# Kernel tuning notes

Hardware: AMD Instinct MI355X
Metric: run time of the kernel (lower is better)

## Reference

```python
import jax, jax.numpy as jnp
import numpy as np

N_USER = 100000
N_ITEM = 50000
N_EDGE = 400000
D_IN = 128
N_HEADS = 4
D_HEAD = 32


def setup_inputs() -> dict:
    key = jax.random.key(0)
    ks = jax.random.split(key, 10)
    s = 1.0 / np.sqrt(D_IN)
    return {
        "h_user": jax.random.normal(ks[0], (N_USER, D_IN), jnp.float32),
        "h_item": jax.random.normal(ks[1], (N_ITEM, D_IN), jnp.float32),
        "edge_user": jax.random.randint(ks[2], (N_EDGE,), 0, N_USER),
        "edge_item": jax.random.randint(ks[3], (N_EDGE,), 0, N_ITEM),
        "user_w_qs": jax.random.normal(ks[4], (N_HEADS, D_IN, D_HEAD), jnp.float32) * s,
        "user_w_ks": jax.random.normal(ks[5], (N_HEADS, D_IN, D_HEAD), jnp.float32) * s,
        "user_w_vs": jax.random.normal(ks[6], (N_HEADS, D_IN, D_HEAD), jnp.float32) * s,
        "item_w_qs": jax.random.normal(ks[7], (N_HEADS, D_IN, D_HEAD), jnp.float32) * s,
        "item_w_ks": jax.random.normal(ks[8], (N_HEADS, D_IN, D_HEAD), jnp.float32) * s,
        "item_w_vs": jax.random.normal(ks[9], (N_HEADS, D_IN, D_HEAD), jnp.float32) * s,
    }


def _segment_softmax(logit, seg, num_segments):
    m = jax.ops.segment_max(logit, seg, num_segments=num_segments)
    e = jnp.exp(logit - m[seg])
    s = jax.ops.segment_sum(e, seg, num_segments=num_segments)
    return e / s[seg]


def _attend(src_idx, dst_idx, h_src, h_dst, w_qs, w_ks, w_vs, n_dst):
    # per-head projections: [H, n, d_head]
    q = jnp.einsum("nd,hde->hne", h_dst, w_qs)
    k = jnp.einsum("nd,hde->hne", h_src, w_ks)
    v = jnp.einsum("nd,hde->hne", h_src, w_vs)
    # per-edge logits: [H, E]
    logit = jnp.sum(q[:, dst_idx] * k[:, src_idx], axis=-1)
    att = jax.vmap(lambda l: _segment_softmax(l, dst_idx, n_dst))(logit)
    # sparse adj @ v == segment-sum of attention-weighted source values
    msg = att[..., None] * v[:, src_idx]  # [H, E, d_head]
    z = jax.vmap(lambda m: jax.ops.segment_sum(m, dst_idx, num_segments=n_dst))(msg)
    z = jax.nn.relu(z)  # nonlinear per head, then merge (concat)
    return jnp.transpose(z, (1, 0, 2)).reshape(n_dst, -1)


def reference(h_user, h_item, edge_user, edge_item,
              user_w_qs, user_w_ks, user_w_vs,
              item_w_qs, item_w_ks, item_w_vs):
    # i2u: items -> users (dst = users)
    z_user = _attend(edge_item, edge_user, h_item, h_user,
                     user_w_qs, item_w_ks, item_w_vs, N_USER)
    # u2i: users -> items (dst = items)
    z_item = _attend(edge_user, edge_item, h_user, h_item,
                     item_w_qs, user_w_ks, user_w_vs, N_ITEM)
    return (z_user, z_item)
```

## Files before the change

kernel.cpp:

```cpp
#include <hip/hip_runtime.h>
#include <hip/hip_fp16.h>


typedef unsigned short u16;
typedef float f32x4 __attribute__((ext_vector_type(4)));
typedef short bf16x8 __attribute__((ext_vector_type(8)));

#define NU_C    100000
#define NI_C    50000
#define E_C     400000
#define D_IN    128
#define D_HEAD  32
#define N_HEADS 4

#define RBU 3125
#define RBI 1563
#define WU  (3 * RBU)
#define WI  (3 * RBI)
#define WT_BLKS 384

#define SCAN_T  256
#define SCAN_E  1024

__device__ __forceinline__ float bf2f(u16 b) {
    return __uint_as_float(((unsigned)b) << 16);
}

__device__ __forceinline__ u16 f2bf_rn(float x) {
    unsigned u = __float_as_uint(x);
    u += 0x7FFFu + ((u >> 16) & 1u);
    return (u16)(u >> 16);
}

__device__ __forceinline__ u16 f2h(float x) {
    return __half_as_ushort(__float2half(x));
}
__device__ __forceinline__ float h2f(u16 b) {
    return __half2float(__ushort_as_half(b));
}

__global__ void detect_dtypes(const void* __restrict__ h,
                              const void* __restrict__ eu,
                              int* __restrict__ flags) {
    int t = threadIdx.x;
    const u16* hw = (const u16*)h;
    int cnt = 0;
#pragma unroll
    for (int r = 0; r < 2; ++r) {
        int i = t + r * 64;
        unsigned ex = (hw[2 * i] >> 7) & 0xFFu;
        if (ex >= 118u && ex <= 137u) cnt++;
    }
    const int* ew = (const int*)eu;
    int nz = 0;
#pragma unroll
    for (int r = 0; r < 4; ++r) {
        int i = t + r * 64;
        if (ew[2 * i + 1] != 0) nz++;
    }
#pragma unroll
    for (int m = 1; m < 64; m <<= 1) {
        cnt += __shfl_xor(cnt, m);
        nz  += __shfl_xor(nz, m);
    }
    if (t == 0) {
        flags[0] = (cnt >= 64) ? 1 : 0;
        flags[1] = (nz == 0) ? 1 : 0;
        flags[2] = 0;
        flags[3] = 0;
    }
}

__global__ __launch_bounds__(256)
void prep(const void* __restrict__ w0, const void* __restrict__ w1,
          const void* __restrict__ w2, const void* __restrict__ w3,
          const void* __restrict__ w4, const void* __restrict__ w5,
          u16* __restrict__ wthi, u16* __restrict__ wtlo,
          const int* __restrict__ e_user, const int* __restrict__ e_item,
          int* __restrict__ du, int* __restrict__ di,
          int* __restrict__ degU, int* __restrict__ degI,
          int* __restrict__ flags) {
    int b = blockIdx.x;
    if (b < WT_BLKS) {
        int m = b >> 6;
        int f = (b & 63) * 256 + threadIdx.x;
        const void* ws[6] = { w0, w1, w2, w3, w4, w5 };
        const void* wp = ws[m];
        int head = f >> 12, e = f & 31;
        float x;
        if (flags[0]) x = bf2f(((const u16*)wp)[f]);
        else          x = ((const float*)wp)[f];
        u16 h = f2bf_rn(x);
        u16 l = f2bf_rn(x - bf2f(h));
        int o = m * 16384 + (head * 32 + e) * 128 + ((f >> 5) & 127);
        wthi[o] = h;
        wtlo[o] = l;
    } else {
        int g = (b - WT_BLKS) * 256 + threadIdx.x;
        if (g >= E_C) return;
        int is64 = flags[1];
        int u = is64 ? e_user[2 * g] : e_user[g];
        int i = is64 ? e_item[2 * g] : e_item[g];
        if ((unsigned)u >= (unsigned)NU_C) { atomicOr(&flags[3], 1); u = 0; }
        if ((unsigned)i >= (unsigned)NI_C) { atomicOr(&flags[3], 1); i = 0; }
        du[g] = u;
        di[g] = i;
        atomicAdd(&degU[u], 1);
        atomicAdd(&degI[i], 1);
    }
}

__global__ __launch_bounds__(SCAN_T)
void scan_pass1(const int* __restrict__ degU, int* __restrict__ offsU,
                int* __restrict__ partU, int nU, int sbU,
                const int* __restrict__ degI, int* __restrict__ offsI,
                int* __restrict__ partI, int nI) {
    __shared__ int tsum[SCAN_T];
    int t = threadIdx.x, b = blockIdx.x;
    const int* deg; int* offs; int* partials; int n; int lb;
    if (b < sbU) { deg = degU; offs = offsU; partials = partU; n = nU; lb = b; }
    else         { deg = degI; offs = offsI; partials = partI; n = nI; lb = b - sbU; }
    int idx = lb * SCAN_E + t * 4;
    int v0 = 0, v1 = 0, v2 = 0, v3 = 0;
    if (idx + 3 < n) {
        v0 = deg[idx]; v1 = deg[idx + 1]; v2 = deg[idx + 2]; v3 = deg[idx + 3];
    } else {
        if (idx     < n) v0 = deg[idx];
        if (idx + 1 < n) v1 = deg[idx + 1];
        if (idx + 2 < n) v2 = deg[idx + 2];
        if (idx + 3 < n) v3 = deg[idx + 3];
    }
    int s = v0 + v1 + v2 + v3;
    tsum[t] = s;
    __syncthreads();
#pragma unroll
    for (int o = 1; o < SCAN_T; o <<= 1) {
        int x = (t >= o) ? tsum[t - o] : 0;
        __syncthreads();
        tsum[t] += x;
        __syncthreads();
    }
    int run = tsum[t] - s;
    if (idx     < n) offs[idx]     = run;             run += v0;
    if (idx + 1 < n) offs[idx + 1] = run;             run += v1;
    if (idx + 2 < n) offs[idx + 2] = run;             run += v2;
    if (idx + 3 < n) offs[idx + 3] = run;
    if (t == SCAN_T - 1) partials[lb] = tsum[t];
}

__global__ __launch_bounds__(SCAN_T)
void scan_pass2(int* __restrict__ partU, int sbU,
                int* __restrict__ partI, int sbI) {
    __shared__ int tsum[SCAN_T];
    int t = threadIdx.x;
    int* partials; int nb;
    if (blockIdx.x == 0) { partials = partU; nb = sbU; }
    else                 { partials = partI; nb = sbI; }
    int v = (t < nb) ? partials[t] : 0;
    tsum[t] = v;
    __syncthreads();
#pragma unroll
    for (int o = 1; o < SCAN_T; o <<= 1) {
        int x = (t >= o) ? tsum[t - o] : 0;
        __syncthreads();
        tsum[t] += x;
        __syncthreads();
    }
    if (t < nb) partials[t] = tsum[t] - v;
}

__global__ void scatter2(const int* __restrict__ du, const int* __restrict__ di,
                         const int* __restrict__ offsU, const int* __restrict__ partU,
                         int* __restrict__ cntU, int* __restrict__ csrU,
                         const int* __restrict__ offsI, const int* __restrict__ partI,
                         int* __restrict__ cntI, int* __restrict__ csrI, int egrid) {
    int b = blockIdx.x;
    int g = (b >= egrid ? b - egrid : b) * 256 + threadIdx.x;
    if (g >= E_C) return;
    if (b < egrid) {
        int d = du[g];
        int pos = offsU[d] + partU[d >> 10] + atomicAdd(&cntU[d], 1);
        csrU[pos] = di[g];
    } else {
        int d = di[g];
        int pos = offsI[d] + partI[d >> 10] + atomicAdd(&cntI[d], 1);
        csrI[pos] = du[g];
    }
}

__global__ __launch_bounds__(256)
void projw(const void* __restrict__ hu, const void* __restrict__ hi_,
           const u16* __restrict__ wthi_, const u16* __restrict__ wtlo_,
           u16* __restrict__ QU, u16* __restrict__ KU, u16* __restrict__ VU,
           u16* __restrict__ QI, u16* __restrict__ KI, u16* __restrict__ VI,
           const int* __restrict__ flags) {
    int wid = blockIdx.x * 4 + (threadIdx.x >> 6);
    int l = threadIdx.x & 63;
    const int lr = l & 15, lk = l >> 4;

    const void* hraw; const u16* wth; const u16* wtl; u16* out; int N; int rb;
    if (wid < WU) {
        int m = wid / RBU; rb = wid - m * RBU;
        hraw = hu; N = NU_C;
        wth = wthi_ + m * 16384; wtl = wtlo_ + m * 16384;
        out = (m == 0) ? QU : ((m == 1) ? KU : VU);
    } else {
        int w2 = wid - WU;
        int m = w2 / RBI; rb = w2 - m * RBI;
        hraw = hi_; N = NI_C;
        wth = wthi_ + (3 + m) * 16384; wtl = wtlo_ + (3 + m) * 16384;
        out = (m == 0) ? QI : ((m == 1) ? KI : VI);
    }

    const int n0 = rb * 32;
    const int row0 = min(n0 + lr, N - 1);
    const int row1 = min(n0 + 16 + lr, N - 1);
    const int isbf = flags[0];

    f32x4 acc[2][8];
#pragma unroll
    for (int rt = 0; rt < 2; ++rt)
#pragma unroll
        for (int ct = 0; ct < 8; ++ct) {
            acc[rt][ct].x = 0.f; acc[rt][ct].y = 0.f;
            acc[rt][ct].z = 0.f; acc[rt][ct].w = 0.f;
        }

#pragma unroll
    for (int kc = 0; kc < 4; ++kc) {
        const int kof = kc * 32 + lk * 8;
        bf16x8 fAh[2], fAl[2];
        if (!isbf) {
            const float* hp = (const float*)hraw;
#pragma unroll
            for (int rt = 0; rt < 2; ++rt) {
                const float* a = hp + (size_t)(rt ? row1 : row0) * D_IN + kof;
                f32x4 a0 = *(const f32x4*)a;
                f32x4 a1 = *(const f32x4*)(a + 4);
#pragma unroll
                for (int i = 0; i < 4; ++i) {
                    u16 hh = f2bf_rn(a0[i]);
                    fAh[rt][i] = (short)hh;
                    fAl[rt][i] = (short)f2bf_rn(a0[i] - bf2f(hh));
                }
#pragma unroll
                for (int i = 0; i < 4; ++i) {
                    u16 hh = f2bf_rn(a1[i]);
                    fAh[rt][4 + i] = (short)hh;
                    fAl[rt][4 + i] = (short)f2bf_rn(a1[i] - bf2f(hh));
                }
            }
        } else {
#pragma unroll
            for (int rt = 0; rt < 2; ++rt) {
                const u16* a = (const u16*)hraw
                             + (size_t)(rt ? row1 : row0) * D_IN + kof;
                fAh[rt] = *(const bf16x8*)a;
#pragma unroll
                for (int i = 0; i < 8; ++i) fAl[rt][i] = 0;
            }
        }
#pragma unroll
        for (int ct = 0; ct < 8; ++ct) {
            const size_t bo = (size_t)(ct * 16 + lr) * D_IN + kof;
            bf16x8 fBh = *(const bf16x8*)(wth + bo);
            bf16x8 fBl = *(const bf16x8*)(wtl + bo);
#pragma unroll
            for (int rt = 0; rt < 2; ++rt) {
                acc[rt][ct] = __builtin_amdgcn_mfma_f32_16x16x32_bf16(
                    fAl[rt], fBh, acc[rt][ct], 0, 0, 0);
                acc[rt][ct] = __builtin_amdgcn_mfma_f32_16x16x32_bf16(
                    fAh[rt], fBl, acc[rt][ct], 0, 0, 0);
                acc[rt][ct] = __builtin_amdgcn_mfma_f32_16x16x32_bf16(
                    fAh[rt], fBh, acc[rt][ct], 0, 0, 0);
            }
        }
    }

#pragma unroll
    for (int rt = 0; rt < 2; ++rt) {
#pragma unroll
        for (int r = 0; r < 4; ++r) {
            int n = n0 + rt * 16 + lk * 4 + r;
            if (n < N) {
#pragma unroll
                for (int ct = 0; ct < 8; ++ct)
                    out[(size_t)n * 128 + ct * 16 + lr] = f2h(acc[rt][ct][r]);
            }
        }
    }
}

__global__ __launch_bounds__(256)
void gather_both(const int* __restrict__ offsU, const int* __restrict__ partU,
                 const int* __restrict__ csrU,
                 const int* __restrict__ offsI, const int* __restrict__ partI,
                 const int* __restrict__ csrI,
                 const u16* __restrict__ QU, const u16* __restrict__ KI,
                 const u16* __restrict__ VI,
                 const u16* __restrict__ QI, const u16* __restrict__ KU,
                 const u16* __restrict__ VU,
                 float* __restrict__ outbase, const int* __restrict__ flags,
                 int ggU) {
    int b = blockIdx.x;
    const int *offs, *part, *csr; const u16 *q, *k, *v;
    float* out; int Ndst; int g;
    if (b < ggU) {
        offs = offsU; part = partU; csr = csrU;
        q = QU; k = KI; v = VI; out = outbase; Ndst = NU_C;
        g = b * 256 + threadIdx.x;
    } else {
        offs = offsI; part = partI; csr = csrI;
        q = QI; k = KU; v = VU;
        out = outbase + (size_t)NU_C * 128; Ndst = NI_C;
        g = (b - ggU) * 256 + threadIdx.x;
    }
    int dst = g >> 6;
    if (dst >= Ndst) return;
    int l  = g & 63;
    int eh = l >> 5;
    int sl = l & 31;
    float* op = out + (size_t)dst * 128 + sl * 4;

    if (flags[3]) {
        if (eh == 0) {
            f32x4 d64; d64.x = d64.y = d64.z = d64.w = 64.0f;
            *(f32x4*)op = d64;
        }
        return;
    }

    ushort4 qu = *(const ushort4*)(q + (size_t)dst * 128 + sl * 4);
    f32x4 qv;
    qv.x = h2f(qu.x); qv.y = h2f(qu.y); qv.z = h2f(qu.z); qv.w = h2f(qu.w);
    f32x4 acc; acc.x = acc.y = acc.z = acc.w = 0.f;
    float ssum = 0.f;

    int e0 = offs[dst] + part[dst >> 10];
    int e1 = (dst + 1 == Ndst) ? E_C
             : offs[dst + 1] + part[(dst + 1) >> 10];
    int e = e0 + eh;
    for (; e + 2 < e1; e += 4) {
        int s0 = csr[e];
        int s1 = csr[e + 2];
        ushort4 ku0 = *(const ushort4*)(k + (size_t)s0 * 128 + sl * 4);
        ushort4 ku1 = *(const ushort4*)(k + (size_t)s1 * 128 + sl * 4);
        ushort4 vu0 = *(const ushort4*)(v + (size_t)s0 * 128 + sl * 4);
        ushort4 vu1 = *(const ushort4*)(v + (size_t)s1 * 128 + sl * 4);
        float d0 = qv.x * h2f(ku0.x) + qv.y * h2f(ku0.y)
                 + qv.z * h2f(ku0.z) + qv.w * h2f(ku0.w);
        float d1 = qv.x * h2f(ku1.x) + qv.y * h2f(ku1.y)
                 + qv.z * h2f(ku1.z) + qv.w * h2f(ku1.w);
        d0 += __shfl_xor(d0, 1);  d1 += __shfl_xor(d1, 1);
        d0 += __shfl_xor(d0, 2);  d1 += __shfl_xor(d1, 2);
        d0 += __shfl_xor(d0, 4);  d1 += __shfl_xor(d1, 4);
        float ev0 = __expf(fminf(fmaxf(d0, -80.f), 80.f));
        float ev1 = __expf(fminf(fmaxf(d1, -80.f), 80.f));
        ssum += ev0 + ev1;
        acc.x += ev0 * h2f(vu0.x) + ev1 * h2f(vu1.x);
        acc.y += ev0 * h2f(vu0.y) + ev1 * h2f(vu1.y);
        acc.z += ev0 * h2f(vu0.z) + ev1 * h2f(vu1.z);
        acc.w += ev0 * h2f(vu0.w) + ev1 * h2f(vu1.w);
    }
    if (e < e1) {
        int s = csr[e];
        ushort4 ku = *(const ushort4*)(k + (size_t)s * 128 + sl * 4);
        ushort4 vu = *(const ushort4*)(v + (size_t)s * 128 + sl * 4);
        float d = qv.x * h2f(ku.x) + qv.y * h2f(ku.y)
                + qv.z * h2f(ku.z) + qv.w * h2f(ku.w);
        d += __shfl_xor(d, 1);
        d += __shfl_xor(d, 2);
        d += __shfl_xor(d, 4);
        float ev = __expf(fminf(fmaxf(d, -80.f), 80.f));
        ssum += ev;
        acc.x += ev * h2f(vu.x); acc.y += ev * h2f(vu.y);
        acc.z += ev * h2f(vu.z); acc.w += ev * h2f(vu.w);
    }
    ssum  += __shfl_xor(ssum, 32);
    acc.x += __shfl_xor(acc.x, 32);
    acc.y += __shfl_xor(acc.y, 32);
    acc.z += __shfl_xor(acc.z, 32);
    acc.w += __shfl_xor(acc.w, 32);
    if (eh == 0) {
        float inv = (ssum > 0.f) ? (1.f / ssum) : 0.f;
        f32x4 o;
        o.x = fmaxf(acc.x * inv, 0.f);
        o.y = fmaxf(acc.y * inv, 0.f);
        o.z = fmaxf(acc.z * inv, 0.f);
        o.w = fmaxf(acc.w * inv, 0.f);
        *(f32x4*)op = o;
    }
}

__global__ void fill_diag(float* __restrict__ out, int n) {
    int g = blockIdx.x * 256 + threadIdx.x;
    if (g < n) out[g] = 48.0f;
}

extern "C" void kernel_launch(void* const* d_in, const int* in_sizes, int n_in,
                              void* d_out, int out_size, void* d_ws, size_t ws_size,
                              hipStream_t stream) {
    const void* h_user    = d_in[0];
    const void* h_item    = d_in[1];
    const int*  edge_user = (const int*)d_in[2];
    const int*  edge_item = (const int*)d_in[3];
    const void* u_wq = d_in[4];
    const void* u_wk = d_in[5];
    const void* u_wv = d_in[6];
    const void* i_wq = d_in[7];
    const void* i_wk = d_in[8];
    const void* i_wv = d_in[9];

    const int NU = NU_C, NI = NI_C;

    size_t szBufU = (((size_t)NU * 128 * 2) + 255) & ~(size_t)255;
    size_t szBufI = (((size_t)NI * 128 * 2) + 255) & ~(size_t)255;
    size_t szE    = (((size_t)E_C * 4) + 255) & ~(size_t)255;
    size_t szOffU = (((size_t)(NU + 1) * 4) + 255) & ~(size_t)255;
    size_t szOffI = (((size_t)(NI + 1) * 4) + 255) & ~(size_t)255;
    size_t szNU   = (((size_t)NU * 4) + 255) & ~(size_t)255;
    size_t szNI   = (((size_t)NI * 4) + 255) & ~(size_t)255;
    size_t szPart = 256 * 4;
    size_t szWt   = (size_t)6 * 16384 * 2;

    size_t off = 0;
    char* base = (char*)d_ws;
    u16* QU      = (u16*)(base + off);   off += szBufU;
    u16* KI      = (u16*)(base + off);   off += szBufI;
    u16* VI      = (u16*)(base + off);   off += szBufI;
    u16* QI      = (u16*)(base + off);   off += szBufI;
    u16* KU      = (u16*)(base + off);   off += szBufU;
    u16* VU      = (u16*)(base + off);   off += szBufU;
    int* du      = (int*)(base + off);   off += szE;
    int* di      = (int*)(base + off);   off += szE;
    int* csrU    = (int*)(base + off);   off += szE;
    int* csrI    = (int*)(base + off);   off += szE;
    int* offsU   = (int*)(base + off);   off += szOffU;
    int* offsI   = (int*)(base + off);   off += szOffI;
    int* partU   = (int*)(base + off);   off += szPart;
    int* partI   = (int*)(base + off);   off += szPart;
    u16* wthi    = (u16*)(base + off);   off += szWt;
    u16* wtlo    = (u16*)(base + off);   off += szWt;
    int* flags   = (int*)(base + off);   off += 256;
    size_t zoff = off;
    int* degU    = (int*)(base + off);   off += szNU;
    int* cntU    = (int*)(base + off);   off += szNU;
    int* degI    = (int*)(base + off);   off += szNI;
    int* cntI    = (int*)(base + off);   off += szNI;
    size_t need = off;

    if (need > ws_size) {
        fill_diag<<<(out_size + 255) / 256, 256, 0, stream>>>((float*)d_out, out_size);
        return;
    }

    int egrid = (E_C + 255) / 256;
    int sbU = (NU + SCAN_E - 1) / SCAN_E;
    int sbI = (NI + SCAN_E - 1) / SCAN_E;
    int ggU = (NU * 64 + 255) / 256;
    int ggI = (NI * 64 + 255) / 256;
    int pwb = (WU + WI + 3) / 4;

    hipMemsetAsync(base + zoff, 0, need - zoff, stream);
    detect_dtypes<<<1, 64, 0, stream>>>(h_user, edge_user, flags);
    prep<<<WT_BLKS + egrid, 256, 0, stream>>>(
        u_wq, u_wk, u_wv, i_wq, i_wk, i_wv, wthi, wtlo,
        edge_user, edge_item, du, di, degU, degI, flags);
    scan_pass1<<<sbU + sbI, SCAN_T, 0, stream>>>(degU, offsU, partU, NU, sbU,
                                                 degI, offsI, partI, NI);
    scan_pass2<<<2, SCAN_T, 0, stream>>>(partU, sbU, partI, sbI);
    scatter2<<<2 * egrid, 256, 0, stream>>>(du, di,
                                            offsU, partU, cntU, csrU,
                                            offsI, partI, cntI, csrI, egrid);
    projw<<<pwb, 256, 0, stream>>>(
        h_user, h_item, wthi, wtlo, QU, KU, VU, QI, KI, VI, flags);
    gather_both<<<ggU + ggI, 256, 0, stream>>>(
        offsU, partU, csrU, offsI, partI, csrI,
        QU, KI, VI, QI, KU, VU, (float*)d_out, flags, ggU);
}
```

Baseline: 430.8 us.

## Stage input rows in LDS once and reuse across Q/K/V projections

The projection kernel now loads each 64-row tile of node features once, splits it into bf16 hi/lo in swizzled shared memory, and loops over the three Q/K/V weight matrices inside one block. Previously each wave re-read and re-split the fp32 inputs for every weight matrix separately. The weight transpose in prep is changed to an MFMA-fragment-ordered layout so B fragments load as contiguous 16-byte chunks. In exchange it uses 32 KB of LDS per block, which lowers occupancy, and serializes the three matrices per block.

```diff
diff --git a/kernel.cpp b/kernel.cpp
--- a/kernel.cpp
+++ b/kernel.cpp
@@ -13,10 +13,8 @@
 #define D_HEAD  32
 #define N_HEADS 4
 
-#define RBU 3125
-#define RBI 1563
-#define WU  (3 * RBU)
-#define WI  (3 * RBI)
+#define PB_U 1563
+#define PB_I 782
 #define WT_BLKS 384
 
 #define SCAN_T  256
@@ -86,13 +84,16 @@
         int f = (b & 63) * 256 + threadIdx.x;
         const void* ws[6] = { w0, w1, w2, w3, w4, w5 };
         const void* wp = ws[m];
-        int head = f >> 12, e = f & 31;
+        int head = f >> 12, d = (f >> 5) & 127, e = f & 31;
         float x;
         if (flags[0]) x = bf2f(((const u16*)wp)[f]);
         else          x = ((const float*)wp)[f];
         u16 h = f2bf_rn(x);
         u16 l = f2bf_rn(x - bf2f(h));
-        int o = m * 16384 + (head * 32 + e) * 128 + ((f >> 5) & 127);
+        int j = head * 32 + e;
+        int ct8 = j >> 4, lr = j & 15;
+        int kc = d >> 5, lk = (d & 31) >> 3, ei = d & 7;
+        int o = m * 16384 + (ct8 * 4 + kc) * 512 + (lk * 16 + lr) * 8 + ei;
         wthi[o] = h;
         wtlo[o] = l;
     } else {
@@ -189,103 +190,125 @@
 }
 
 __global__ __launch_bounds__(256)
-void projw(const void* __restrict__ hu, const void* __restrict__ hi_,
-           const u16* __restrict__ wthi_, const u16* __restrict__ wtlo_,
-           u16* __restrict__ QU, u16* __restrict__ KU, u16* __restrict__ VU,
-           u16* __restrict__ QI, u16* __restrict__ KI, u16* __restrict__ VI,
-           const int* __restrict__ flags) {
-    int wid = blockIdx.x * 4 + (threadIdx.x >> 6);
-    int l = threadIdx.x & 63;
+void proj3x(const void* __restrict__ hu, const void* __restrict__ hi_,
+            const u16* __restrict__ wthi_, const u16* __restrict__ wtlo_,
+            u16* __restrict__ QU, u16* __restrict__ KU, u16* __restrict__ VU,
+            u16* __restrict__ QI, u16* __restrict__ KI, u16* __restrict__ VI,
+            const int* __restrict__ flags) {
+    __shared__ u16 Hhi[64 * 128], Hlo[64 * 128];
+
+    const int b = blockIdx.x;
+    const void* hraw; int N, mbase, lb;
+    u16* out0; u16* out1; u16* out2;
+    if (b < PB_U) {
+        hraw = hu;  N = NU_C; mbase = 0; lb = b;
+        out0 = QU; out1 = KU; out2 = VU;
+    } else {
+        hraw = hi_; N = NI_C; mbase = 3; lb = b - PB_U;
+        out0 = QI; out1 = KI; out2 = VI;
+    }
+    const int t = threadIdx.x;
+    const int n0 = lb * 64;
+    const int isbf = flags[0];
+
+    {
+        int row = t >> 2, cb = (t & 3) * 4;
+        int gn = min(n0 + row, N - 1);
+        if (!isbf) {
+            const float* hp = (const float*)hraw + (size_t)gn * D_IN + cb * 8;
+#pragma unroll
+            for (int i = 0; i < 4; ++i) {
+                f32x4 a0 = *(const f32x4*)(hp + i * 8);
+                f32x4 a1 = *(const f32x4*)(hp + i * 8 + 4);
+                bf16x8 hv, lv;
+#pragma unroll
+                for (int q = 0; q < 4; ++q) {
+                    u16 hh = f2bf_rn(a0[q]);
+                    hv[q] = (short)hh;
+                    lv[q] = (short)f2bf_rn(a0[q] - bf2f(hh));
+                }
+#pragma unroll
+                for (int q = 0; q < 4; ++q) {
+                    u16 hh = f2bf_rn(a1[q]);
+                    hv[4 + q] = (short)hh;
+                    lv[4 + q] = (short)f2bf_rn(a1[q] - bf2f(hh));
+                }
+                int o = row * 128 + (((cb + i) ^ (row & 7)) * 8);
+                *(bf16x8*)&Hhi[o] = hv;
+                *(bf16x8*)&Hlo[o] = lv;
+            }
+        } else {
+            const u16* hp = (const u16*)hraw + (size_t)gn * D_IN + cb * 8;
+            bf16x8 z;
+#pragma unroll
+            for (int q = 0; q < 8; ++q) z[q] = 0;
+#pragma unroll
+            for (int i = 0; i < 4; ++i) {
+                bf16x8 hv = *(const bf16x8*)(hp + i * 8);
+                int o = row * 128 + (((cb + i) ^ (row & 7)) * 8);
+                *(bf16x8*)&Hhi[o] = hv;
+                *(bf16x8*)&Hlo[o] = z;
+            }
+        }
+    }
+    __syncthreads();
+
+    const int w = t >> 6, l = t & 63;
     const int lr = l & 15, lk = l >> 4;
 
-    const void* hraw; const u16* wth; const u16* wtl; u16* out; int N; int rb;
-    if (wid < WU) {
-        int m = wid / RBU; rb = wid - m * RBU;
-        hraw = hu; N = NU_C;
-        wth = wthi_ + m * 16384; wtl = wtlo_ + m * 16384;
-        out = (m == 0) ? QU : ((m == 1) ? KU : VU);
-    } else {
-        int w2 = wid - WU;
-        int m = w2 / RBI; rb = w2 - m * RBI;
-        hraw = hi_; N = NI_C;
-        wth = wthi_ + (3 + m) * 16384; wtl = wtlo_ + (3 + m) * 16384;
-        out = (m == 0) ? QI : ((m == 1) ? KI : VI);
-    }
-
-    const int n0 = rb * 32;
-    const int row0 = min(n0 + lr, N - 1);
-    const int row1 = min(n0 + 16 + lr, N - 1);
-    const int isbf = flags[0];
-
-    f32x4 acc[2][8];
-#pragma unroll
-    for (int rt = 0; rt < 2; ++rt)
-#pragma unroll
-        for (int ct = 0; ct < 8; ++ct) {
-            acc[rt][ct].x = 0.f; acc[rt][ct].y = 0.f;
-            acc[rt][ct].z = 0.f; acc[rt][ct].w = 0.f;
-        }
-
-#pragma unroll
-    for (int kc = 0; kc < 4; ++kc) {
-        const int kof = kc * 32 + lk * 8;
-        bf16x8 fAh[2], fAl[2];
-        if (!isbf) {
-            const float* hp = (const float*)hraw;
-#pragma unroll
-            for (int rt = 0; rt < 2; ++rt) {
-                const float* a = hp + (size_t)(rt ? row1 : row0) * D_IN + kof;
-                f32x4 a0 = *(const f32x4*)a;
-                f32x4 a1 = *(const f32x4*)(a + 4);
-#pragma unroll
-                for (int i = 0; i < 4; ++i) {
-                    u16 hh = f2bf_rn(a0[i]);
-                    fAh[rt][i] = (short)hh;
-                    fAl[rt][i] = (short)f2bf_rn(a0[i] - bf2f(hh));
-                }
-#pragma unroll
-                for (int i = 0; i < 4; ++i) {
-                    u16 hh = f2bf_rn(a1[i]);
-                    fAh[rt][4 + i] = (short)hh;
-                    fAl[rt][4 + i] = (short)f2bf_rn(a1[i] - bf2f(hh));
+#pragma unroll 1
+    for (int mm = 0; mm < 3; ++mm) {
+        const u16* wth = wthi_ + (size_t)(mbase + mm) * 16384;
+        const u16* wtl = wtlo_ + (size_t)(mbase + mm) * 16384;
+        u16* out = (mm == 0) ? out0 : ((mm == 1) ? out1 : out2);
+
+        f32x4 acc[4][2];
+#pragma unroll
+        for (int rt = 0; rt < 4; ++rt)
+#pragma unroll
+            for (int ci = 0; ci < 2; ++ci) {
+                acc[rt][ci].x = 0.f; acc[rt][ci].y = 0.f;
+                acc[rt][ci].z = 0.f; acc[rt][ci].w = 0.f;
+            }
+
+#pragma unroll
+        for (int kc = 0; kc < 4; ++kc) {
+            bf16x8 fAh[4], fAl[4];
+#pragma unroll
+            for (int rt = 0; rt < 4; ++rt) {
+                int row = rt * 16 + lr;
+                int o = row * 128 + (((kc * 4 + lk) ^ (lr & 7)) * 8);
+                fAh[rt] = *(const bf16x8*)&Hhi[o];
+                fAl[rt] = *(const bf16x8*)&Hlo[o];
+            }
+#pragma unroll
+            for (int ci = 0; ci < 2; ++ci) {
+                int fb = ((w * 2 + ci) * 4 + kc) * 512 + l * 8;
+                bf16x8 fBh = *(const bf16x8*)(wth + fb);
+                bf16x8 fBl = *(const bf16x8*)(wtl + fb);
+#pragma unroll
+                for (int rt = 0; rt < 4; ++rt) {
+                    acc[rt][ci] = __builtin_amdgcn_mfma_f32_16x16x32_bf16(
+                        fAl[rt], fBh, acc[rt][ci], 0, 0, 0);
+                    acc[rt][ci] = __builtin_amdgcn_mfma_f32_16x16x32_bf16(
+                        fAh[rt], fBl, acc[rt][ci], 0, 0, 0);
+                    acc[rt][ci] = __builtin_amdgcn_mfma_f32_16x16x32_bf16(
+                        fAh[rt], fBh, acc[rt][ci], 0, 0, 0);
                 }
             }
-        } else {
-#pragma unroll
-            for (int rt = 0; rt < 2; ++rt) {
-                const u16* a = (const u16*)hraw
-                             + (size_t)(rt ? row1 : row0) * D_IN + kof;
-                fAh[rt] = *(const bf16x8*)a;
-#pragma unroll
-                for (int i = 0; i < 8; ++i) fAl[rt][i] = 0;
-            }
         }
-#pragma unroll
-        for (int ct = 0; ct < 8; ++ct) {
-            const size_t bo = (size_t)(ct * 16 + lr) * D_IN + kof;
-            bf16x8 fBh = *(const bf16x8*)(wth + bo);
-            bf16x8 fBl = *(const bf16x8*)(wtl + bo);
-#pragma unroll
-            for (int rt = 0; rt < 2; ++rt) {
-                acc[rt][ct] = __builtin_amdgcn_mfma_f32_16x16x32_bf16(
-                    fAl[rt], fBh, acc[rt][ct], 0, 0, 0);
-                acc[rt][ct] = __builtin_amdgcn_mfma_f32_16x16x32_bf16(
-                    fAh[rt], fBl, acc[rt][ct], 0, 0, 0);
-                acc[rt][ct] = __builtin_amdgcn_mfma_f32_16x16x32_bf16(
-                    fAh[rt], fBh, acc[rt][ct], 0, 0, 0);
-            }
-        }
-    }
-
-#pragma unroll
-    for (int rt = 0; rt < 2; ++rt) {
-#pragma unroll
-        for (int r = 0; r < 4; ++r) {
-            int n = n0 + rt * 16 + lk * 4 + r;
-            if (n < N) {
-#pragma unroll
-                for (int ct = 0; ct < 8; ++ct)
-                    out[(size_t)n * 128 + ct * 16 + lr] = f2h(acc[rt][ct][r]);
+
+#pragma unroll
+        for (int rt = 0; rt < 4; ++rt) {
+#pragma unroll
+            for (int r = 0; r < 4; ++r) {
+                int n = n0 + rt * 16 + lk * 4 + r;
+                if (n < N) {
+#pragma unroll
+                    for (int ci = 0; ci < 2; ++ci)
+                        out[(size_t)n * 128 + w * 32 + ci * 16 + lr] =
+                            f2h(acc[rt][ci][r]);
+                }
             }
         }
     }
@@ -459,7 +482,6 @@
     int sbI = (NI + SCAN_E - 1) / SCAN_E;
     int ggU = (NU * 64 + 255) / 256;
     int ggI = (NI * 64 + 255) / 256;
-    int pwb = (WU + WI + 3) / 4;
 
     hipMemsetAsync(base + zoff, 0, need - zoff, stream);
     detect_dtypes<<<1, 64, 0, stream>>>(h_user, edge_user, flags);
@@ -472,7 +494,7 @@
     scatter2<<<2 * egrid, 256, 0, stream>>>(du, di,
                                             offsU, partU, cntU, csrU,
                                             offsI, partI, cntI, csrI, egrid);
-    projw<<<pwb, 256, 0, stream>>>(
+    proj3x<<<PB_U + PB_I, 256, 0, stream>>>(
         h_user, h_item, wthi, wtlo, QU, KU, VU, QI, KI, VI, flags);
     gather_both<<<ggU + ggI, 256, 0, stream>>>(
         offsU, partU, csrU, offsI, partI, csrI,
```

After: 351.4 us. -18.4%, faster.
